# Kernel tuning notes

Hardware: AMD Instinct MI355X
Metric: run time of the kernel (lower is better)

## Reference

```python
import jax, jax.numpy as jnp
import numpy as np

N = 50000      # nodes
E = 800000     # edges (avg degree 16)
F_IN = 64      # node_features (== GENConv out, so no input projection)
H = 64         # hidden
EXP = 2 * H    # GENConv MLP expansion dim = 128
D2 = F_IN + H  # dense-block concat dim = SAGEConv in = 128
EPS_MSG = 1e-7 # GENConv message eps
BN_EPS = 1e-5


def setup_inputs() -> dict:
    key = jax.random.key(0)
    ks = jax.random.split(key, 16)
    g = lambda k, shape, fan: jax.random.normal(k, shape, jnp.float32) / np.sqrt(fan)
    return {
        "x": jax.random.normal(ks[0], (N, F_IN), jnp.float32),
        "edge_index": jax.random.randint(ks[1], (2, E), 0, N, jnp.int32),
        # GENConv MLP: Linear(64,128) -> BatchNorm(128) -> ReLU -> Linear(128,64)
        "W1": g(ks[2], (H, EXP), H), "b1": jnp.zeros((EXP,), jnp.float32),
        "gamma": jnp.ones((EXP,), jnp.float32), "beta": jnp.zeros((EXP,), jnp.float32),
        "W2": g(ks[3], (EXP, H), EXP), "b2": jnp.zeros((H,), jnp.float32),
        # SAGEConv project Linear(128,128), lin_l Linear(128,64), lin_r Linear(128,64,bias=False)
        "Wp": g(ks[4], (D2, D2), D2), "bp": jnp.zeros((D2,), jnp.float32),
        "Wl": g(ks[5], (D2, H), D2), "bl": jnp.zeros((H,), jnp.float32),
        "Wr": g(ks[6], (D2, H), D2),
        # fc Linear(64,1)
        "Wf": g(ks[7], (H, 1), H), "bf": jnp.zeros((1,), jnp.float32),
    }


def _forward(x, W1, b1, gamma, beta, W2, b2, Wp, bp, Wl, bl, Wr, Wf, bf, src, dst):
    n = x.shape[0]
    # ---- GENConv(aggr='softmax', t=1.0): msg = relu(x_j) + eps -------------
    msg = jax.nn.relu(x[src]) + EPS_MSG                       # [E, H]
    mmax = jax.ops.segment_max(msg, dst, num_segments=n)      # per-dst, per-feature max
    mmax = jax.lax.stop_gradient(jnp.where(jnp.isfinite(mmax), mmax, 0.0))
    e = jnp.exp(msg - mmax[dst])                              # t = 1.0
    denom = jax.ops.segment_sum(e, dst, num_segments=n)
    numer = jax.ops.segment_sum(e * msg, dst, num_segments=n)
    agg = numer / jnp.where(denom > 0, denom, 1.0)            # softmax aggregation
    out = agg + x                                             # residual with x_dst
    # GENConv MLP (BatchNorm in training mode: batch stats, biased var)
    h = out @ W1 + b1
    mu = h.mean(axis=0)
    var = h.var(axis=0)
    h = (h - mu) * jax.lax.rsqrt(var + BN_EPS) * gamma + beta
    h = jax.nn.relu(h) @ W2 + b2                              # [N, H]
    # ---- DeepGCNLayer block='dense': concat input ---------------------------
    x2 = jnp.concatenate([x, h], axis=-1)                     # [N, F_IN+H]
    x2 = jax.nn.sigmoid(x2)                                   # self.relu = Sigmoid()
    # ---- SAGEConv(project=True, aggr=DeepSetsAggregation()==sum) -----------
    xp = jax.nn.relu(x2 @ Wp + bp)                            # projected source feats
    aggr = jax.ops.segment_sum(xp[src], dst, num_segments=n)  # DeepSets w/o nns = sum
    out2 = aggr @ Wl + bl + x2 @ Wr                           # root uses UNprojected x2
    out2 = jax.nn.sigmoid(out2)
    logits = out2 @ Wf + bf                                   # [N, 1]
    probs = jax.nn.sigmoid(logits)                            # training branch
    return probs, logits


def reference(x, edge_index, W1, b1, gamma, beta, W2, b2, Wp, bp, Wl, bl, Wr, Wf, bf):
    src, dst = edge_index[0], edge_index[1]
    return _forward(x, W1, b1, gamma, beta, W2, b2, Wp, bp, Wl, bl, Wr, Wf, bf, src, dst)
```

## Files before the change

kernel.cpp:

```cpp
#include <hip/hip_runtime.h>

#define F_IN 64
#define HID 64
#define EXPD 128
#define D2 128
#define MAXDEG 64
#define NBW 128
#define NB 391
#define BINCAP 2400
#define EPT 32

typedef __attribute__((ext_vector_type(8))) short bf16x8;
typedef __attribute__((ext_vector_type(4))) float f32x4;

__device__ __forceinline__ float sigmoidf_(float x) {
    return 1.0f / (1.0f + __expf(-x));
}
__device__ __forceinline__ unsigned bf16rne_(float f) {
    unsigned u = __float_as_uint(f);
    return (u + 0x7FFFu + ((u >> 16) & 1u)) >> 16;
}
__device__ __forceinline__ float bf16tof_(unsigned u16) {
    return __uint_as_float(u16 << 16);
}

__global__ __launch_bounds__(256) void k_bin(const int* __restrict__ ei,
                                             int* __restrict__ binCount,
                                             unsigned* __restrict__ binned,
                                             const float* __restrict__ x,
                                             unsigned short* __restrict__ x16,
                                             const float* __restrict__ W1,
                                             const float* __restrict__ W2,
                                             const float* __restrict__ Wp,
                                             const float* __restrict__ Wl,
                                             const float* __restrict__ Wr,
                                             short* __restrict__ dst,
                                             int nE, int n, int nbinb) {
    int b = blockIdx.x;
    if (b < nbinb) {
        __shared__ int hist[NB];
        __shared__ int base[NB];
        int tid = threadIdx.x;
        for (int i = tid; i < NB; i += 256) hist[i] = 0;
        __syncthreads();
        unsigned ed[EPT];
        unsigned short rk[EPT];
        int e0 = b * (256 * EPT);
#pragma unroll
        for (int j = 0; j < EPT; ++j) {
            int e = e0 + j * 256 + tid;
            if (e < nE) {
                unsigned s = (unsigned)ei[e];
                unsigned d = (unsigned)ei[nE + e];
                ed[j] = s | (d << 16);
                rk[j] = (unsigned short)atomicAdd(&hist[d >> 7], 1);
            }
        }
        __syncthreads();
        for (int i = tid; i < NB; i += 256) {
            int h = hist[i];
            base[i] = h > 0 ? atomicAdd(&binCount[i], h) : 0;
        }
        __syncthreads();
#pragma unroll
        for (int j = 0; j < EPT; ++j) {
            int e = e0 + j * 256 + tid;
            if (e < nE) {
                int bin = (ed[j] >> 16) >> 7;
                int pos = base[bin] + (int)rk[j];
                if (pos < BINCAP) binned[(size_t)bin * BINCAP + pos] = ed[j];
            }
        }
        return;
    }
    b -= nbinb;
    if (b < 192) {
        int e = b * 256 + threadIdx.x;
        const float* src;
        int K, N, base2;
        if (e < 8192)       { src = W1; K = 64;  N = 128; base2 = 0; }
        else if (e < 16384) { src = W2; K = 128; N = 64;  base2 = 8192; }
        else if (e < 32768) { src = Wp; K = 128; N = 128; base2 = 16384; }
        else if (e < 40960) { src = Wl; K = 128; N = 64;  base2 = 32768; }
        else                { src = Wr; K = 128; N = 64;  base2 = 40960; }
        int le = e - base2;
        int j = le & 7;
        int lane = (le >> 3) & 63;
        int n16 = lane & 15, q = lane >> 4;
        int rest = le >> 9;
        int KC = K / 32;
        int kc = rest % KC, nt = rest / KC;
        int k = kc * 32 + q * 8 + j;
        int col = nt * 16 + n16;
        dst[e] = (short)bf16rne_(src[(size_t)k * N + col]);
        return;
    }
    int i0 = (b - 192) * 1024 + threadIdx.x * 4;
    if (i0 < n * F_IN) {
        float4 v = *(const float4*)(x + i0);
        uint2 pk;
        pk.x = bf16rne_(v.x) | (bf16rne_(v.y) << 16);
        pk.y = bf16rne_(v.z) | (bf16rne_(v.w) << 16);
        *(uint2*)(x16 + i0) = pk;
    }
}

__global__ __launch_bounds__(256) void k_csr(const int* __restrict__ binCount,
                                             const unsigned* __restrict__ binned,
                                             int* __restrict__ counts,
                                             unsigned short* __restrict__ csr, int n) {
    __shared__ unsigned short lcsr[NBW * MAXDEG];
    __shared__ int lcnt[NBW];
    int b = blockIdx.x;
    int tid = threadIdx.x;
    if (tid < NBW) lcnt[tid] = 0;
    __syncthreads();
    int cnt = binCount[b];
    cnt = cnt < BINCAP ? cnt : BINCAP;
    const unsigned* src = binned + (size_t)b * BINCAP;
    for (int i = tid; i < cnt; i += 256) {
        unsigned u = src[i];
        int dl = (int)(u >> 16) - b * NBW;
        int slot = atomicAdd(&lcnt[dl], 1);
        if (slot < MAXDEG) lcsr[dl * MAXDEG + slot] = (unsigned short)(u & 0xFFFF);
    }
    __syncthreads();
    int nodebase = b * NBW;
    if (tid < NBW && nodebase + tid < n) counts[nodebase + tid] = lcnt[tid];
    int nrows = n - nodebase;
    nrows = nrows < NBW ? nrows : NBW;
    int nu4 = nrows * 8;
    uint4* dstrow = (uint4*)(csr + (size_t)nodebase * MAXDEG);
    for (int idx = tid; idx < nu4; idx += 256) dstrow[idx] = ((const uint4*)lcsr)[idx];
}

__global__ __launch_bounds__(256) void k_gen(const unsigned short* __restrict__ x16,
                                             const int* __restrict__ counts,
                                             const unsigned short* __restrict__ csr,
                                             unsigned short* __restrict__ gen16, int n) {
    const unsigned* x32 = (const unsigned*)x16;
    int wid = threadIdx.x >> 6;
    int lane = threadIdx.x & 63;
    int H = lane >> 5, f2 = lane & 31;
    int v = blockIdx.x * 4 + wid;
    if (v >= n) return;
    int deg = counts[v];
    deg = deg > MAXDEG ? MAXDEG : deg;
    int idx = 0;
    if (lane < deg) idx = (int)csr[(size_t)v * MAXDEG + lane];
    float d0 = 0.f, d1 = 0.f, n0 = 0.f, n1 = 0.f;
    int i = 0;
    for (; i + 8 <= deg; i += 8) {
        int sA = __shfl(idx, i + 0 + H, 64);
        int sB = __shfl(idx, i + 2 + H, 64);
        int sC = __shfl(idx, i + 4 + H, 64);
        int sD = __shfl(idx, i + 6 + H, 64);
        unsigned uA = x32[(size_t)sA * 32 + f2];
        unsigned uB = x32[(size_t)sB * 32 + f2];
        unsigned uC = x32[(size_t)sC * 32 + f2];
        unsigned uD = x32[(size_t)sD * 32 + f2];
#pragma unroll
        for (int t = 0; t < 4; ++t) {
            unsigned u = t == 0 ? uA : t == 1 ? uB : t == 2 ? uC : uD;
            float m0 = fmaxf(bf16tof_(u & 0xFFFF), 0.f) + 1e-7f;
            float m1 = fmaxf(bf16tof_(u >> 16), 0.f) + 1e-7f;
            float e0 = __expf(m0), e1 = __expf(m1);
            d0 += e0; d1 += e1;
            n0 = fmaf(e0, m0, n0);
            n1 = fmaf(e1, m1, n1);
        }
    }
    for (; i + 2 <= deg; i += 2) {
        int s = __shfl(idx, i + H, 64);
        unsigned u = x32[(size_t)s * 32 + f2];
        float m0 = fmaxf(bf16tof_(u & 0xFFFF), 0.f) + 1e-7f;
        float m1 = fmaxf(bf16tof_(u >> 16), 0.f) + 1e-7f;
        float e0 = __expf(m0), e1 = __expf(m1);
        d0 += e0; d1 += e1;
        n0 = fmaf(e0, m0, n0);
        n1 = fmaf(e1, m1, n1);
    }
    if (i < deg) {
        int s = __shfl(idx, i, 64);
        if (H == 0) {
            unsigned u = x32[(size_t)s * 32 + f2];
            float m0 = fmaxf(bf16tof_(u & 0xFFFF), 0.f) + 1e-7f;
            float m1 = fmaxf(bf16tof_(u >> 16), 0.f) + 1e-7f;
            float e0 = __expf(m0), e1 = __expf(m1);
            d0 += e0; d1 += e1;
            n0 = fmaf(e0, m0, n0);
            n1 = fmaf(e1, m1, n1);
        }
    }
    d0 += __shfl_xor(d0, 32, 64);
    d1 += __shfl_xor(d1, 32, 64);
    n0 += __shfl_xor(n0, 32, 64);
    n1 += __shfl_xor(n1, 32, 64);
    if (H == 0) {
        float a0 = (deg > 0) ? (n0 / d0) : 0.f;
        float a1 = (deg > 0) ? (n1 / d1) : 0.f;
        unsigned xv = x32[(size_t)v * 32 + f2];
        float r0 = a0 + bf16tof_(xv & 0xFFFF);
        float r1 = a1 + bf16tof_(xv >> 16);
        ((unsigned*)gen16)[(size_t)v * 32 + f2] =
            bf16rne_(r0) | (bf16rne_(r1) << 16);
    }
}

__global__ __launch_bounds__(256) void k_gemm1(const unsigned short* __restrict__ gen16,
                                               const short* __restrict__ Wf,
                                               const float* __restrict__ b1,
                                               unsigned short* __restrict__ h16,
                                               float* __restrict__ bnsums, int n) {
    __shared__ short As[64 * 64];
    __shared__ float bnred[256];
    int tid = threadIdx.x;
    int rblk = blockIdx.x * 64;
    if (tid < 256) bnred[tid] = 0.f;
#pragma unroll
    for (int it = 0; it < 2; ++it) {
        int c = it * 256 + tid;
        int rr = c & 63, q8 = c >> 6;
        int gr = rblk + rr;
        gr = gr < n ? gr : n - 1;
        uint4 v = *(const uint4*)(gen16 + (size_t)gr * F_IN + q8 * 8);
        int slot = ((rr >> 4) * 2 + (q8 >> 2)) * 64 + (q8 & 3) * 16 + (rr & 15);
        *(uint4*)(As + slot * 8) = v;
    }
    __syncthreads();
    int L = tid & 63, w = tid >> 6;
    int q = L >> 4, n16 = L & 15;
    int mt_base = (w & 1) * 2;
    int nt_base = (w >> 1) * 4;
    f32x4 acc[2][4];
#pragma unroll
    for (int mt = 0; mt < 2; ++mt)
#pragma unroll
        for (int nt = 0; nt < 4; ++nt) acc[mt][nt] = (f32x4){0.f, 0.f, 0.f, 0.f};
#pragma unroll
    for (int kc = 0; kc < 2; ++kc) {
        bf16x8 a0 = *(const bf16x8*)(As + (((mt_base + 0) * 2 + kc) * 64 + L) * 8);
        bf16x8 a1 = *(const bf16x8*)(As + (((mt_base + 1) * 2 + kc) * 64 + L) * 8);
#pragma unroll
        for (int nt = 0; nt < 4; ++nt) {
            bf16x8 b = *(const bf16x8*)(Wf + (size_t)(((nt_base + nt) * 2 + kc) * 64 + L) * 8);
            acc[0][nt] = __builtin_amdgcn_mfma_f32_16x16x32_bf16(a0, b, acc[0][nt], 0, 0, 0);
            acc[1][nt] = __builtin_amdgcn_mfma_f32_16x16x32_bf16(a1, b, acc[1][nt], 0, 0, 0);
        }
    }
#pragma unroll
    for (int nt = 0; nt < 4; ++nt) {
        int col = (nt_base + nt) * 16 + n16;
        float bv = b1[col];
        float s = 0.f, s2 = 0.f;
#pragma unroll
        for (int mt = 0; mt < 2; ++mt)
#pragma unroll
            for (int r = 0; r < 4; ++r) {
                int row = rblk + (w & 1) * 32 + mt * 16 + q * 4 + r;
                float hv = acc[mt][nt][r] + bv;
                if (row < n) {
                    h16[(size_t)row * EXPD + col] = (unsigned short)bf16rne_(hv);
                    s += hv;
                    s2 = fmaf(hv, hv, s2);
                }
            }
        s += __shfl_xor(s, 16, 64);
        s += __shfl_xor(s, 32, 64);
        s2 += __shfl_xor(s2, 16, 64);
        s2 += __shfl_xor(s2, 32, 64);
        if (q == 0) {
            atomicAdd(&bnred[col], s);
            atomicAdd(&bnred[128 + col], s2);
        }
    }
    __syncthreads();
    if (tid < 256) atomicAdd(&bnsums[tid], bnred[tid]);
}

__global__ __launch_bounds__(256) void k_mlp2a(const unsigned short* __restrict__ h16,
                                               const float* __restrict__ bnsums,
                                               const float* __restrict__ gamma,
                                               const float* __restrict__ beta,
                                               const short* __restrict__ Wf,
                                               const float* __restrict__ b2,
                                               const unsigned short* __restrict__ x16,
                                               unsigned short* __restrict__ x2_16,
                                               float inv_n, int n) {
    __shared__ short As[128 * 128];
    __shared__ float ssl[256];
    int tid = threadIdx.x;
    int rblk = blockIdx.x * 128;
    if (tid < 128) {
        float mu = bnsums[tid] * inv_n;
        float var = fmaf(-mu, mu, bnsums[128 + tid] * inv_n);
        float rs = rsqrtf(fmaxf(var, 0.f) + 1e-5f);
        float scale = gamma[tid] * rs;
        ssl[tid] = scale;
        ssl[128 + tid] = fmaf(-mu, scale, beta[tid]);
    }
    __syncthreads();
#pragma unroll
    for (int it = 0; it < 8; ++it) {
        int c = it * 256 + tid;
        int rr = c & 127, q8 = c >> 7;
        int gr = rblk + rr;
        gr = gr < n ? gr : n - 1;
        uint4 v = *(const uint4*)(h16 + (size_t)gr * EXPD + q8 * 8);
        float4 sc1 = *(const float4*)(ssl + q8 * 8);
        float4 sc2 = *(const float4*)(ssl + q8 * 8 + 4);
        float4 sh1 = *(const float4*)(ssl + 128 + q8 * 8);
        float4 sh2 = *(const float4*)(ssl + 128 + q8 * 8 + 4);
        float o0 = fmaxf(fmaf(bf16tof_(v.x & 0xFFFF), sc1.x, sh1.x), 0.f);
        float o1 = fmaxf(fmaf(bf16tof_(v.x >> 16),    sc1.y, sh1.y), 0.f);
        float o2 = fmaxf(fmaf(bf16tof_(v.y & 0xFFFF), sc1.z, sh1.z), 0.f);
        float o3 = fmaxf(fmaf(bf16tof_(v.y >> 16),    sc1.w, sh1.w), 0.f);
        float o4 = fmaxf(fmaf(bf16tof_(v.z & 0xFFFF), sc2.x, sh2.x), 0.f);
        float o5 = fmaxf(fmaf(bf16tof_(v.z >> 16),    sc2.y, sh2.y), 0.f);
        float o6 = fmaxf(fmaf(bf16tof_(v.w & 0xFFFF), sc2.z, sh2.z), 0.f);
        float o7 = fmaxf(fmaf(bf16tof_(v.w >> 16),    sc2.w, sh2.w), 0.f);
        uint4 pk;
        pk.x = bf16rne_(o0) | (bf16rne_(o1) << 16);
        pk.y = bf16rne_(o2) | (bf16rne_(o3) << 16);
        pk.z = bf16rne_(o4) | (bf16rne_(o5) << 16);
        pk.w = bf16rne_(o6) | (bf16rne_(o7) << 16);
        int slot = ((rr >> 4) * 4 + (q8 >> 2)) * 64 + (q8 & 3) * 16 + (rr & 15);
        *(uint4*)(As + slot * 8) = pk;
    }
    __syncthreads();
    int L = tid & 63, w = tid >> 6;
    int q = L >> 4, n16 = L & 15;
    int mt_base = w * 2;
    f32x4 acc[2][4];
#pragma unroll
    for (int mt = 0; mt < 2; ++mt)
#pragma unroll
        for (int nt = 0; nt < 4; ++nt) acc[mt][nt] = (f32x4){0.f, 0.f, 0.f, 0.f};
#pragma unroll
    for (int kc = 0; kc < 4; ++kc) {
        bf16x8 a0 = *(const bf16x8*)(As + (((mt_base + 0) * 4 + kc) * 64 + L) * 8);
        bf16x8 a1 = *(const bf16x8*)(As + (((mt_base + 1) * 4 + kc) * 64 + L) * 8);
#pragma unroll
        for (int nt = 0; nt < 4; ++nt) {
            bf16x8 b = *(const bf16x8*)(Wf + (size_t)((nt * 4 + kc) * 64 + L) * 8);
            acc[0][nt] = __builtin_amdgcn_mfma_f32_16x16x32_bf16(a0, b, acc[0][nt], 0, 0, 0);
            acc[1][nt] = __builtin_amdgcn_mfma_f32_16x16x32_bf16(a1, b, acc[1][nt], 0, 0, 0);
        }
    }
#pragma unroll
    for (int it = 0; it < 8; ++it) {
        int i = it * 256 + tid;
        int rr = i >> 4, c4 = i & 15;
        int row = rblk + rr;
        if (row < n) {
            uint2 xv = ((const uint2*)x16)[(size_t)row * 16 + c4];
            float s0 = sigmoidf_(bf16tof_(xv.x & 0xFFFF));
            float s1 = sigmoidf_(bf16tof_(xv.x >> 16));
            float s2 = sigmoidf_(bf16tof_(xv.y & 0xFFFF));
            float s3 = sigmoidf_(bf16tof_(xv.y >> 16));
            uint2 pk;
            pk.x = bf16rne_(s0) | (bf16rne_(s1) << 16);
            pk.y = bf16rne_(s2) | (bf16rne_(s3) << 16);
            *(uint2*)(x2_16 + (size_t)row * D2 + c4 * 4) = pk;
        }
    }
#pragma unroll
    for (int nt = 0; nt < 4; ++nt) {
        int col = nt * 16 + n16;
        float bv = b2[col];
#pragma unroll
        for (int mt = 0; mt < 2; ++mt)
#pragma unroll
            for (int r = 0; r < 4; ++r) {
                int row = rblk + w * 32 + mt * 16 + q * 4 + r;
                if (row < n)
                    x2_16[(size_t)row * D2 + 64 + col] =
                        (unsigned short)bf16rne_(sigmoidf_(acc[mt][nt][r] + bv));
            }
    }
}

__global__ __launch_bounds__(256) void k_mlp2b(const unsigned short* __restrict__ x2_16,
                                               const short* __restrict__ Wfp,
                                               const short* __restrict__ Wfl,
                                               const float* __restrict__ bp,
                                               unsigned short* __restrict__ yp16, int n) {
    __shared__ short As[64 * 128];
    int tid = threadIdx.x;
    int rblk = blockIdx.x * 64;
#pragma unroll
    for (int it = 0; it < 4; ++it) {
        int c = it * 256 + tid;
        int rr = c & 63, q8 = c >> 6;
        int gr = rblk + rr;
        gr = gr < n ? gr : n - 1;
        uint4 v = *(const uint4*)(x2_16 + (size_t)gr * D2 + q8 * 8);
        int slot = ((rr >> 4) * 4 + (q8 >> 2)) * 64 + (q8 & 3) * 16 + (rr & 15);
        *(uint4*)(As + slot * 8) = v;
    }
    __syncthreads();
    int L = tid & 63, w = tid >> 6;
    int q = L >> 4, n16 = L & 15;
    int mt_base = (w & 1) * 2;
    int nt_base = (w >> 1) * 4;
    f32x4 acc[2][4];
#pragma unroll
    for (int mt = 0; mt < 2; ++mt)
#pragma unroll
        for (int nt = 0; nt < 4; ++nt) acc[mt][nt] = (f32x4){0.f, 0.f, 0.f, 0.f};
#pragma unroll
    for (int kc = 0; kc < 4; ++kc) {
        bf16x8 a0 = *(const bf16x8*)(As + (((mt_base + 0) * 4 + kc) * 64 + L) * 8);
        bf16x8 a1 = *(const bf16x8*)(As + (((mt_base + 1) * 4 + kc) * 64 + L) * 8);
#pragma unroll
        for (int nt = 0; nt < 4; ++nt) {
            bf16x8 b = *(const bf16x8*)(Wfp + (size_t)(((nt_base + nt) * 4 + kc) * 64 + L) * 8);
            acc[0][nt] = __builtin_amdgcn_mfma_f32_16x16x32_bf16(a0, b, acc[0][nt], 0, 0, 0);
            acc[1][nt] = __builtin_amdgcn_mfma_f32_16x16x32_bf16(a1, b, acc[1][nt], 0, 0, 0);
        }
    }
    __syncthreads();
#pragma unroll
    for (int nt = 0; nt < 4; ++nt) {
        int kk = (nt_base + nt) * 16 + n16;
        float bv = bp[kk];
        int q8b = kk >> 3, jb = kk & 7;
#pragma unroll
        for (int mt = 0; mt < 2; ++mt)
#pragma unroll
            for (int r = 0; r < 4; ++r) {
                int rr2 = (w & 1) * 32 + mt * 16 + q * 4 + r;
                float xv = fmaxf(acc[mt][nt][r] + bv, 0.f);
                int slot = ((rr2 >> 4) * 4 + (q8b >> 2)) * 64 + (q8b & 3) * 16 + (rr2 & 15);
                As[slot * 8 + jb] = (short)bf16rne_(xv);
            }
    }
    __syncthreads();
    f32x4 acc2[4];
#pragma unroll
    for (int nt = 0; nt < 4; ++nt) acc2[nt] = (f32x4){0.f, 0.f, 0.f, 0.f};
#pragma unroll
    for (int kc = 0; kc < 4; ++kc) {
        bf16x8 a = *(const bf16x8*)(As + ((w * 4 + kc) * 64 + L) * 8);
#pragma unroll
        for (int nt = 0; nt < 4; ++nt) {
            bf16x8 b = *(const bf16x8*)(Wfl + (size_t)((nt * 4 + kc) * 64 + L) * 8);
            acc2[nt] = __builtin_amdgcn_mfma_f32_16x16x32_bf16(a, b, acc2[nt], 0, 0, 0);
        }
    }
#pragma unroll
    for (int nt = 0; nt < 4; ++nt) {
        int col = nt * 16 + n16;
#pragma unroll
        for (int r = 0; r < 4; ++r) {
            int row = rblk + w * 16 + q * 4 + r;
            if (row < n)
                yp16[(size_t)row * HID + col] = (unsigned short)bf16rne_(acc2[nt][r]);
        }
    }
}

__global__ __launch_bounds__(256) void k_sage(const unsigned short* __restrict__ yp16,
                                              const int* __restrict__ counts,
                                              const unsigned short* __restrict__ csr,
                                              unsigned short* __restrict__ aggr16, int n) {
    const unsigned* yp32 = (const unsigned*)yp16;
    int wid = threadIdx.x >> 6;
    int lane = threadIdx.x & 63;
    int H = lane >> 5, f2 = lane & 31;
    int v = blockIdx.x * 4 + wid;
    if (v >= n) return;
    int deg = counts[v];
    deg = deg > MAXDEG ? MAXDEG : deg;
    int idx = 0;
    if (lane < deg) idx = (int)csr[(size_t)v * MAXDEG + lane];
    float a0 = 0.f, a1 = 0.f;
    int i = 0;
    for (; i + 8 <= deg; i += 8) {
        int sA = __shfl(idx, i + 0 + H, 64);
        int sB = __shfl(idx, i + 2 + H, 64);
        int sC = __shfl(idx, i + 4 + H, 64);
        int sD = __shfl(idx, i + 6 + H, 64);
        unsigned uA = yp32[(size_t)sA * 32 + f2];
        unsigned uB = yp32[(size_t)sB * 32 + f2];
        unsigned uC = yp32[(size_t)sC * 32 + f2];
        unsigned uD = yp32[(size_t)sD * 32 + f2];
        a0 += bf16tof_(uA & 0xFFFF) + bf16tof_(uB & 0xFFFF) +
              bf16tof_(uC & 0xFFFF) + bf16tof_(uD & 0xFFFF);
        a1 += bf16tof_(uA >> 16) + bf16tof_(uB >> 16) +
              bf16tof_(uC >> 16) + bf16tof_(uD >> 16);
    }
    for (; i + 2 <= deg; i += 2) {
        int s = __shfl(idx, i + H, 64);
        unsigned u = yp32[(size_t)s * 32 + f2];
        a0 += bf16tof_(u & 0xFFFF);
        a1 += bf16tof_(u >> 16);
    }
    if (i < deg) {
        int s = __shfl(idx, i, 64);
        if (H == 0) {
            unsigned u = yp32[(size_t)s * 32 + f2];
            a0 += bf16tof_(u & 0xFFFF);
            a1 += bf16tof_(u >> 16);
        }
    }
    a0 += __shfl_xor(a0, 32, 64);
    a1 += __shfl_xor(a1, 32, 64);
    if (H == 0)
        ((unsigned*)aggr16)[(size_t)v * 32 + f2] = bf16rne_(a0) | (bf16rne_(a1) << 16);
}

__global__ __launch_bounds__(256) void k_final(const unsigned short* __restrict__ aggr16,
                                               const unsigned short* __restrict__ x2_16,
                                               const short* __restrict__ Wfr,
                                               const float* __restrict__ bl,
                                               const float* __restrict__ Wfv,
                                               const float* __restrict__ bf,
                                               float* __restrict__ out, int n) {
    __shared__ short As[128 * 128];
    int tid = threadIdx.x;
    int rblk = blockIdx.x * 128;
#pragma unroll
    for (int it = 0; it < 8; ++it) {
        int c = it * 256 + tid;
        int rr = c & 127, q8 = c >> 7;
        int gr = rblk + rr;
        gr = gr < n ? gr : n - 1;
        uint4 v = *(const uint4*)(x2_16 + (size_t)gr * D2 + q8 * 8);
        int slot = ((rr >> 4) * 4 + (q8 >> 2)) * 64 + (q8 & 3) * 16 + (rr & 15);
        *(uint4*)(As + slot * 8) = v;
    }
    __syncthreads();
    int L = tid & 63, w = tid >> 6;
    int q = L >> 4, n16 = L & 15;
    int mt_base = w * 2;
    f32x4 acc[2][4];
#pragma unroll
    for (int mt = 0; mt < 2; ++mt)
#pragma unroll
        for (int nt = 0; nt < 4; ++nt) acc[mt][nt] = (f32x4){0.f, 0.f, 0.f, 0.f};
#pragma unroll
    for (int kc = 0; kc < 4; ++kc) {
        bf16x8 a0 = *(const bf16x8*)(As + (((mt_base + 0) * 4 + kc) * 64 + L) * 8);
        bf16x8 a1 = *(const bf16x8*)(As + (((mt_base + 1) * 4 + kc) * 64 + L) * 8);
#pragma unroll
        for (int nt = 0; nt < 4; ++nt) {
            bf16x8 b = *(const bf16x8*)(Wfr + (size_t)((nt * 4 + kc) * 64 + L) * 8);
            acc[0][nt] = __builtin_amdgcn_mfma_f32_16x16x32_bf16(a0, b, acc[0][nt], 0, 0, 0);
            acc[1][nt] = __builtin_amdgcn_mfma_f32_16x16x32_bf16(a1, b, acc[1][nt], 0, 0, 0);
        }
    }
    float blv[4], wfv[4];
#pragma unroll
    for (int nt = 0; nt < 4; ++nt) {
        blv[nt] = bl[nt * 16 + n16];
        wfv[nt] = Wfv[nt * 16 + n16];
    }
    float bf0 = bf[0];
#pragma unroll
    for (int mt = 0; mt < 2; ++mt)
#pragma unroll
        for (int r = 0; r < 4; ++r) {
            int row = rblk + w * 32 + mt * 16 + q * 4 + r;
            int rowc = row < n ? row : n - 1;
            float t = 0.f;
#pragma unroll
            for (int nt = 0; nt < 4; ++nt) {
                float ag = bf16tof_(aggr16[(size_t)rowc * HID + nt * 16 + n16]);
                t = fmaf(sigmoidf_(acc[mt][nt][r] + blv[nt] + ag), wfv[nt], t);
            }
            t += __shfl_xor(t, 1, 64);
            t += __shfl_xor(t, 2, 64);
            t += __shfl_xor(t, 4, 64);
            t += __shfl_xor(t, 8, 64);
            if (n16 == 0 && row < n) {
                float lg = t + bf0;
                out[row] = sigmoidf_(lg);
                out[n + row] = lg;
            }
        }
}

extern "C" void kernel_launch(void* const* d_in, const int* in_sizes, int n_in,
                              void* d_out, int out_size, void* d_ws, size_t ws_size,
                              hipStream_t stream) {
    const float* x     = (const float*)d_in[0];
    const int*   ei    = (const int*)d_in[1];
    const float* W1    = (const float*)d_in[2];
    const float* b1    = (const float*)d_in[3];
    const float* gamma = (const float*)d_in[4];
    const float* beta  = (const float*)d_in[5];
    const float* W2    = (const float*)d_in[6];
    const float* b2    = (const float*)d_in[7];
    const float* Wp    = (const float*)d_in[8];
    const float* bp    = (const float*)d_in[9];
    const float* Wl    = (const float*)d_in[10];
    const float* bl    = (const float*)d_in[11];
    const float* Wr    = (const float*)d_in[12];
    const float* Wfv   = (const float*)d_in[13];
    const float* bf    = (const float*)d_in[14];
    const int n = in_sizes[0] / F_IN;
    const int e = in_sizes[1] / 2;

    char* ws = (char*)d_ws;
    size_t off = 0;
    auto alloc = [&](size_t bytes) -> void* {
        void* p = (void*)(ws + off);
        off += (bytes + 255) & ~(size_t)255;
        return p;
    };
    float*          bnsums   = (float*)alloc(256 * 4 + NB * 4);
    int*            binCount = (int*)((char*)bnsums + 1024);
    int*            counts   = (int*)alloc((size_t)n * 4);
    unsigned short* csr      = (unsigned short*)alloc((size_t)n * MAXDEG * 2);
    unsigned*       binned   = (unsigned*)alloc((size_t)NB * BINCAP * 4);
    unsigned short* x16      = (unsigned short*)alloc((size_t)n * F_IN * 2);
    unsigned short* gen16    = (unsigned short*)alloc((size_t)n * F_IN * 2);
    unsigned short* h16      = (unsigned short*)alloc((size_t)n * EXPD * 2);
    unsigned short* x2_16    = (unsigned short*)alloc((size_t)n * D2 * 2);
    unsigned short* yp16     = (unsigned short*)alloc((size_t)n * HID * 2);
    unsigned short* aggr16   = (unsigned short*)alloc((size_t)n * HID * 2);
    short*          wfrag    = (short*)alloc(49152 * 2);

    float* out = (float*)d_out;
    const int nb64  = (n + 63) / 64;
    const int nb128 = (n + 127) / 128;
    const int nb4   = (n + 3) / 4;
    const int nbinb = (e + 256 * EPT - 1) / (256 * EPT);
    const int nfp = nbinb + 192 + ((n * F_IN + 1023) / 1024);

    hipMemsetAsync(bnsums, 0, 1024 + NB * 4, stream);

    k_bin<<<nfp, 256, 0, stream>>>(ei, binCount, binned, x, x16, W1, W2, Wp, Wl,
                                   Wr, wfrag, e, n, nbinb);
    k_csr<<<NB, 256, 0, stream>>>(binCount, binned, counts, csr, n);
    k_gen<<<nb4, 256, 0, stream>>>(x16, counts, csr, gen16, n);
    k_gemm1<<<nb64, 256, 0, stream>>>(gen16, wfrag, b1, h16, bnsums, n);
    k_mlp2a<<<nb128, 256, 0, stream>>>(h16, bnsums, gamma, beta, wfrag + 8192, b2,
                                       x16, x2_16, 1.0f / (float)n, n);
    k_mlp2b<<<nb64, 256, 0, stream>>>(x2_16, wfrag + 16384, wfrag + 32768, bp,
                                      yp16, n);
    k_sage<<<nb4, 256, 0, stream>>>(yp16, counts, csr, aggr16, n);
    k_final<<<nb128, 256, 0, stream>>>(aggr16, x2_16, wfrag + 40960, bl, Wfv, bf,
                                       out, n);
}
```

Measured before the change: 232.7 us.

## Fuse GENConv aggregation into GEMM1 and merge MLP2 with SAGE projection

The softmax gather-aggregation is moved into the first GEMM kernel, so each block aggregates its 64 rows straight into shared memory and the gen16 round trip through global memory goes away. The second MLP GEMM, the sigmoid concat and the SAGE projection/lin_l GEMMs are merged into one kernel that keeps x2 in shared memory instead of re-reading it. This removes two launches and intermediate traffic. The cost is fewer blocks doing the gather (64 rows per block with 16 serial nodes per wave) and a larger per-block register and LDS footprint, which may reduce latency hiding.

```diff
diff --git a/kernel.cpp b/kernel.cpp
--- a/kernel.cpp
+++ b/kernel.cpp
@@ -134,55 +134,52 @@
     for (int idx = tid; idx < nu4; idx += 256) dstrow[idx] = ((const uint4*)lcsr)[idx];
 }
 
-__global__ __launch_bounds__(256) void k_gen(const unsigned short* __restrict__ x16,
-                                             const int* __restrict__ counts,
-                                             const unsigned short* __restrict__ csr,
-                                             unsigned short* __restrict__ gen16, int n) {
+__global__ __launch_bounds__(256) void k_gengemm1(const unsigned short* __restrict__ x16,
+                                                  const int* __restrict__ counts,
+                                                  const unsigned short* __restrict__ csr,
+                                                  const short* __restrict__ Wf,
+                                                  const float* __restrict__ b1,
+                                                  unsigned short* __restrict__ h16,
+                                                  float* __restrict__ bnsums, int n) {
+    __shared__ short As[64 * 64];
+    __shared__ float bnred[256];
     const unsigned* x32 = (const unsigned*)x16;
-    int wid = threadIdx.x >> 6;
-    int lane = threadIdx.x & 63;
-    int H = lane >> 5, f2 = lane & 31;
-    int v = blockIdx.x * 4 + wid;
-    if (v >= n) return;
-    int deg = counts[v];
-    deg = deg > MAXDEG ? MAXDEG : deg;
-    int idx = 0;
-    if (lane < deg) idx = (int)csr[(size_t)v * MAXDEG + lane];
-    float d0 = 0.f, d1 = 0.f, n0 = 0.f, n1 = 0.f;
-    int i = 0;
-    for (; i + 8 <= deg; i += 8) {
-        int sA = __shfl(idx, i + 0 + H, 64);
-        int sB = __shfl(idx, i + 2 + H, 64);
-        int sC = __shfl(idx, i + 4 + H, 64);
-        int sD = __shfl(idx, i + 6 + H, 64);
-        unsigned uA = x32[(size_t)sA * 32 + f2];
-        unsigned uB = x32[(size_t)sB * 32 + f2];
-        unsigned uC = x32[(size_t)sC * 32 + f2];
-        unsigned uD = x32[(size_t)sD * 32 + f2];
-#pragma unroll
-        for (int t = 0; t < 4; ++t) {
-            unsigned u = t == 0 ? uA : t == 1 ? uB : t == 2 ? uC : uD;
-            float m0 = fmaxf(bf16tof_(u & 0xFFFF), 0.f) + 1e-7f;
-            float m1 = fmaxf(bf16tof_(u >> 16), 0.f) + 1e-7f;
-            float e0 = __expf(m0), e1 = __expf(m1);
-            d0 += e0; d1 += e1;
-            n0 = fmaf(e0, m0, n0);
-            n1 = fmaf(e1, m1, n1);
-        }
-    }
-    for (; i + 2 <= deg; i += 2) {
-        int s = __shfl(idx, i + H, 64);
-        unsigned u = x32[(size_t)s * 32 + f2];
-        float m0 = fmaxf(bf16tof_(u & 0xFFFF), 0.f) + 1e-7f;
-        float m1 = fmaxf(bf16tof_(u >> 16), 0.f) + 1e-7f;
-        float e0 = __expf(m0), e1 = __expf(m1);
-        d0 += e0; d1 += e1;
-        n0 = fmaf(e0, m0, n0);
-        n1 = fmaf(e1, m1, n1);
-    }
-    if (i < deg) {
-        int s = __shfl(idx, i, 64);
-        if (H == 0) {
+    int tid = threadIdx.x;
+    int rblk = blockIdx.x * 64;
+    if (tid < 256) bnred[tid] = 0.f;
+    int L = tid & 63, w = tid >> 6;
+    int H = L >> 5, f2 = L & 31;
+    for (int t = 0; t < 16; ++t) {
+        int vv = rblk + w * 16 + t;
+        int v = vv < n ? vv : n - 1;
+        int deg = counts[v];
+        deg = deg > MAXDEG ? MAXDEG : deg;
+        int idx = 0;
+        if (L < deg) idx = (int)csr[(size_t)v * MAXDEG + L];
+        float d0 = 0.f, d1 = 0.f, n0 = 0.f, n1 = 0.f;
+        int i = 0;
+        for (; i + 8 <= deg; i += 8) {
+            int sA = __shfl(idx, i + 0 + H, 64);
+            int sB = __shfl(idx, i + 2 + H, 64);
+            int sC = __shfl(idx, i + 4 + H, 64);
+            int sD = __shfl(idx, i + 6 + H, 64);
+            unsigned uA = x32[(size_t)sA * 32 + f2];
+            unsigned uB = x32[(size_t)sB * 32 + f2];
+            unsigned uC = x32[(size_t)sC * 32 + f2];
+            unsigned uD = x32[(size_t)sD * 32 + f2];
+#pragma unroll
+            for (int tt = 0; tt < 4; ++tt) {
+                unsigned u = tt == 0 ? uA : tt == 1 ? uB : tt == 2 ? uC : uD;
+                float m0 = fmaxf(bf16tof_(u & 0xFFFF), 0.f) + 1e-7f;
+                float m1 = fmaxf(bf16tof_(u >> 16), 0.f) + 1e-7f;
+                float e0 = __expf(m0), e1 = __expf(m1);
+                d0 += e0; d1 += e1;
+                n0 = fmaf(e0, m0, n0);
+                n1 = fmaf(e1, m1, n1);
+            }
+        }
+        for (; i + 2 <= deg; i += 2) {
+            int s = __shfl(idx, i + H, 64);
             unsigned u = x32[(size_t)s * 32 + f2];
             float m0 = fmaxf(bf16tof_(u & 0xFFFF), 0.f) + 1e-7f;
             float m1 = fmaxf(bf16tof_(u >> 16), 0.f) + 1e-7f;
@@ -191,44 +188,35 @@
             n0 = fmaf(e0, m0, n0);
             n1 = fmaf(e1, m1, n1);
         }
-    }
-    d0 += __shfl_xor(d0, 32, 64);
-    d1 += __shfl_xor(d1, 32, 64);
-    n0 += __shfl_xor(n0, 32, 64);
-    n1 += __shfl_xor(n1, 32, 64);
-    if (H == 0) {
-        float a0 = (deg > 0) ? (n0 / d0) : 0.f;
-        float a1 = (deg > 0) ? (n1 / d1) : 0.f;
-        unsigned xv = x32[(size_t)v * 32 + f2];
-        float r0 = a0 + bf16tof_(xv & 0xFFFF);
-        float r1 = a1 + bf16tof_(xv >> 16);
-        ((unsigned*)gen16)[(size_t)v * 32 + f2] =
-            bf16rne_(r0) | (bf16rne_(r1) << 16);
-    }
-}
-
-__global__ __launch_bounds__(256) void k_gemm1(const unsigned short* __restrict__ gen16,
-                                               const short* __restrict__ Wf,
-                                               const float* __restrict__ b1,
-                                               unsigned short* __restrict__ h16,
-                                               float* __restrict__ bnsums, int n) {
-    __shared__ short As[64 * 64];
-    __shared__ float bnred[256];
-    int tid = threadIdx.x;
-    int rblk = blockIdx.x * 64;
-    if (tid < 256) bnred[tid] = 0.f;
-#pragma unroll
-    for (int it = 0; it < 2; ++it) {
-        int c = it * 256 + tid;
-        int rr = c & 63, q8 = c >> 6;
-        int gr = rblk + rr;
-        gr = gr < n ? gr : n - 1;
-        uint4 v = *(const uint4*)(gen16 + (size_t)gr * F_IN + q8 * 8);
-        int slot = ((rr >> 4) * 2 + (q8 >> 2)) * 64 + (q8 & 3) * 16 + (rr & 15);
-        *(uint4*)(As + slot * 8) = v;
-    }
-    __syncthreads();
-    int L = tid & 63, w = tid >> 6;
+        if (i < deg) {
+            int s = __shfl(idx, i, 64);
+            if (H == 0) {
+                unsigned u = x32[(size_t)s * 32 + f2];
+                float m0 = fmaxf(bf16tof_(u & 0xFFFF), 0.f) + 1e-7f;
+                float m1 = fmaxf(bf16tof_(u >> 16), 0.f) + 1e-7f;
+                float e0 = __expf(m0), e1 = __expf(m1);
+                d0 += e0; d1 += e1;
+                n0 = fmaf(e0, m0, n0);
+                n1 = fmaf(e1, m1, n1);
+            }
+        }
+        d0 += __shfl_xor(d0, 32, 64);
+        d1 += __shfl_xor(d1, 32, 64);
+        n0 += __shfl_xor(n0, 32, 64);
+        n1 += __shfl_xor(n1, 32, 64);
+        if (H == 0) {
+            float a0 = (deg > 0) ? (n0 / d0) : 0.f;
+            float a1 = (deg > 0) ? (n1 / d1) : 0.f;
+            unsigned xv = x32[(size_t)v * 32 + f2];
+            float r0 = a0 + bf16tof_(xv & 0xFFFF);
+            float r1 = a1 + bf16tof_(xv >> 16);
+            int q8 = f2 >> 2;
+            int j = (2 * f2) & 7;
+            int slot = (w * 2 + (q8 >> 2)) * 64 + (q8 & 3) * 16 + t;
+            *(unsigned*)(As + slot * 8 + j) = bf16rne_(r0) | (bf16rne_(r1) << 16);
+        }
+    }
+    __syncthreads();
     int q = L >> 4, n16 = L & 15;
     int mt_base = (w & 1) * 2;
     int nt_base = (w >> 1) * 4;
@@ -278,15 +266,19 @@
     if (tid < 256) atomicAdd(&bnsums[tid], bnred[tid]);
 }
 
-__global__ __launch_bounds__(256) void k_mlp2a(const unsigned short* __restrict__ h16,
-                                               const float* __restrict__ bnsums,
-                                               const float* __restrict__ gamma,
-                                               const float* __restrict__ beta,
-                                               const short* __restrict__ Wf,
-                                               const float* __restrict__ b2,
-                                               const unsigned short* __restrict__ x16,
-                                               unsigned short* __restrict__ x2_16,
-                                               float inv_n, int n) {
+__global__ __launch_bounds__(256) void k_mlp2(const unsigned short* __restrict__ h16,
+                                              const float* __restrict__ bnsums,
+                                              const float* __restrict__ gamma,
+                                              const float* __restrict__ beta,
+                                              const short* __restrict__ Wf2,
+                                              const float* __restrict__ b2,
+                                              const unsigned short* __restrict__ x16,
+                                              const short* __restrict__ Wfp,
+                                              const short* __restrict__ Wfl,
+                                              const float* __restrict__ bp,
+                                              unsigned short* __restrict__ x2_16,
+                                              unsigned short* __restrict__ yp16,
+                                              float inv_n, int n) {
     __shared__ short As[128 * 128];
     __shared__ float ssl[256];
     int tid = threadIdx.x;
@@ -330,7 +322,6 @@
     __syncthreads();
     int L = tid & 63, w = tid >> 6;
     int q = L >> 4, n16 = L & 15;
-    int mt_base = w * 2;
     f32x4 acc[2][4];
 #pragma unroll
     for (int mt = 0; mt < 2; ++mt)
@@ -338,125 +329,114 @@
         for (int nt = 0; nt < 4; ++nt) acc[mt][nt] = (f32x4){0.f, 0.f, 0.f, 0.f};
 #pragma unroll
     for (int kc = 0; kc < 4; ++kc) {
-        bf16x8 a0 = *(const bf16x8*)(As + (((mt_base + 0) * 4 + kc) * 64 + L) * 8);
-        bf16x8 a1 = *(const bf16x8*)(As + (((mt_base + 1) * 4 + kc) * 64 + L) * 8);
+        bf16x8 a0 = *(const bf16x8*)(As + (((w * 2 + 0) * 4 + kc) * 64 + L) * 8);
+        bf16x8 a1 = *(const bf16x8*)(As + (((w * 2 + 1) * 4 + kc) * 64 + L) * 8);
 #pragma unroll
         for (int nt = 0; nt < 4; ++nt) {
-            bf16x8 b = *(const bf16x8*)(Wf + (size_t)((nt * 4 + kc) * 64 + L) * 8);
+            bf16x8 b = *(const bf16x8*)(Wf2 + (size_t)((nt * 4 + kc) * 64 + L) * 8);
             acc[0][nt] = __builtin_amdgcn_mfma_f32_16x16x32_bf16(a0, b, acc[0][nt], 0, 0, 0);
             acc[1][nt] = __builtin_amdgcn_mfma_f32_16x16x32_bf16(a1, b, acc[1][nt], 0, 0, 0);
         }
     }
+    __syncthreads();
 #pragma unroll
     for (int it = 0; it < 8; ++it) {
         int i = it * 256 + tid;
         int rr = i >> 4, c4 = i & 15;
-        int row = rblk + rr;
-        if (row < n) {
-            uint2 xv = ((const uint2*)x16)[(size_t)row * 16 + c4];
-            float s0 = sigmoidf_(bf16tof_(xv.x & 0xFFFF));
-            float s1 = sigmoidf_(bf16tof_(xv.x >> 16));
-            float s2 = sigmoidf_(bf16tof_(xv.y & 0xFFFF));
-            float s3 = sigmoidf_(bf16tof_(xv.y >> 16));
-            uint2 pk;
-            pk.x = bf16rne_(s0) | (bf16rne_(s1) << 16);
-            pk.y = bf16rne_(s2) | (bf16rne_(s3) << 16);
-            *(uint2*)(x2_16 + (size_t)row * D2 + c4 * 4) = pk;
-        }
+        int gr = rblk + rr;
+        int grc = gr < n ? gr : n - 1;
+        uint2 xv = ((const uint2*)x16)[(size_t)grc * 16 + c4];
+        float s0 = sigmoidf_(bf16tof_(xv.x & 0xFFFF));
+        float s1 = sigmoidf_(bf16tof_(xv.x >> 16));
+        float s2 = sigmoidf_(bf16tof_(xv.y & 0xFFFF));
+        float s3 = sigmoidf_(bf16tof_(xv.y >> 16));
+        uint2 pk;
+        pk.x = bf16rne_(s0) | (bf16rne_(s1) << 16);
+        pk.y = bf16rne_(s2) | (bf16rne_(s3) << 16);
+        if (gr < n) *(uint2*)(x2_16 + (size_t)gr * D2 + c4 * 4) = pk;
+        int q8 = c4 >> 1, j = (c4 & 1) * 4;
+        int slot = ((rr >> 4) * 4 + (q8 >> 2)) * 64 + (q8 & 3) * 16 + (rr & 15);
+        *(uint2*)(As + slot * 8 + j) = pk;
     }
 #pragma unroll
     for (int nt = 0; nt < 4; ++nt) {
         int col = nt * 16 + n16;
         float bv = b2[col];
+        int kk = 64 + col;
+        int q8b = kk >> 3, jb = kk & 7;
 #pragma unroll
         for (int mt = 0; mt < 2; ++mt)
 #pragma unroll
             for (int r = 0; r < 4; ++r) {
-                int row = rblk + w * 32 + mt * 16 + q * 4 + r;
+                int rr2 = w * 32 + mt * 16 + q * 4 + r;
+                int row = rblk + rr2;
+                unsigned sv = bf16rne_(sigmoidf_(acc[mt][nt][r] + bv));
                 if (row < n)
-                    x2_16[(size_t)row * D2 + 64 + col] =
-                        (unsigned short)bf16rne_(sigmoidf_(acc[mt][nt][r] + bv));
-            }
-    }
-}
-
-__global__ __launch_bounds__(256) void k_mlp2b(const unsigned short* __restrict__ x2_16,
-                                               const short* __restrict__ Wfp,
-                                               const short* __restrict__ Wfl,
-                                               const float* __restrict__ bp,
-                                               unsigned short* __restrict__ yp16, int n) {
-    __shared__ short As[64 * 128];
-    int tid = threadIdx.x;
-    int rblk = blockIdx.x * 64;
-#pragma unroll
-    for (int it = 0; it < 4; ++it) {
-        int c = it * 256 + tid;
-        int rr = c & 63, q8 = c >> 6;
-        int gr = rblk + rr;
-        gr = gr < n ? gr : n - 1;
-        uint4 v = *(const uint4*)(x2_16 + (size_t)gr * D2 + q8 * 8);
-        int slot = ((rr >> 4) * 4 + (q8 >> 2)) * 64 + (q8 & 3) * 16 + (rr & 15);
-        *(uint4*)(As + slot * 8) = v;
-    }
-    __syncthreads();
-    int L = tid & 63, w = tid >> 6;
-    int q = L >> 4, n16 = L & 15;
-    int mt_base = (w & 1) * 2;
-    int nt_base = (w >> 1) * 4;
-    f32x4 acc[2][4];
+                    x2_16[(size_t)row * D2 + 64 + col] = (unsigned short)sv;
+                int slot = ((rr2 >> 4) * 4 + (q8b >> 2)) * 64 + (q8b & 3) * 16 + (rr2 & 15);
+                As[slot * 8 + jb] = (short)sv;
+            }
+    }
+    __syncthreads();
+    f32x4 accp[2][8];
 #pragma unroll
     for (int mt = 0; mt < 2; ++mt)
 #pragma unroll
-        for (int nt = 0; nt < 4; ++nt) acc[mt][nt] = (f32x4){0.f, 0.f, 0.f, 0.f};
+        for (int nt = 0; nt < 8; ++nt) accp[mt][nt] = (f32x4){0.f, 0.f, 0.f, 0.f};
 #pragma unroll
     for (int kc = 0; kc < 4; ++kc) {
-        bf16x8 a0 = *(const bf16x8*)(As + (((mt_base + 0) * 4 + kc) * 64 + L) * 8);
-        bf16x8 a1 = *(const bf16x8*)(As + (((mt_base + 1) * 4 + kc) * 64 + L) * 8);
-#pragma unroll
-        for (int nt = 0; nt < 4; ++nt) {
-            bf16x8 b = *(const bf16x8*)(Wfp + (size_t)(((nt_base + nt) * 4 + kc) * 64 + L) * 8);
-            acc[0][nt] = __builtin_amdgcn_mfma_f32_16x16x32_bf16(a0, b, acc[0][nt], 0, 0, 0);
-            acc[1][nt] = __builtin_amdgcn_mfma_f32_16x16x32_bf16(a1, b, acc[1][nt], 0, 0, 0);
-        }
-    }
-    __syncthreads();
-#pragma unroll
-    for (int nt = 0; nt < 4; ++nt) {
-        int kk = (nt_base + nt) * 16 + n16;
-        float bv = bp[kk];
-        int q8b = kk >> 3, jb = kk & 7;
+        bf16x8 a0 = *(const bf16x8*)(As + (((w * 2 + 0) * 4 + kc) * 64 + L) * 8);
+        bf16x8 a1 = *(const bf16x8*)(As + (((w * 2 + 1) * 4 + kc) * 64 + L) * 8);
+#pragma unroll
+        for (int nt = 0; nt < 8; ++nt) {
+            bf16x8 b = *(const bf16x8*)(Wfp + (size_t)((nt * 4 + kc) * 64 + L) * 8);
+            accp[0][nt] = __builtin_amdgcn_mfma_f32_16x16x32_bf16(a0, b, accp[0][nt], 0, 0, 0);
+            accp[1][nt] = __builtin_amdgcn_mfma_f32_16x16x32_bf16(a1, b, accp[1][nt], 0, 0, 0);
+        }
+    }
+#pragma unroll
+    for (int nt = 0; nt < 8; ++nt) {
+        int col = nt * 16 + n16;
+        float bv = bp[col];
+        int q8b = col >> 3, jb = col & 7;
 #pragma unroll
         for (int mt = 0; mt < 2; ++mt)
 #pragma unroll
             for (int r = 0; r < 4; ++r) {
-                int rr2 = (w & 1) * 32 + mt * 16 + q * 4 + r;
-                float xv = fmaxf(acc[mt][nt][r] + bv, 0.f);
+                int rr2 = (w * 2 + mt) * 16 + q * 4 + r;
+                float xv = fmaxf(accp[mt][nt][r] + bv, 0.f);
                 int slot = ((rr2 >> 4) * 4 + (q8b >> 2)) * 64 + (q8b & 3) * 16 + (rr2 & 15);
                 As[slot * 8 + jb] = (short)bf16rne_(xv);
             }
     }
-    __syncthreads();
-    f32x4 acc2[4];
-#pragma unroll
-    for (int nt = 0; nt < 4; ++nt) acc2[nt] = (f32x4){0.f, 0.f, 0.f, 0.f};
+    f32x4 acc2[2][4];
+#pragma unroll
+    for (int mt = 0; mt < 2; ++mt)
+#pragma unroll
+        for (int nt = 0; nt < 4; ++nt) acc2[mt][nt] = (f32x4){0.f, 0.f, 0.f, 0.f};
 #pragma unroll
     for (int kc = 0; kc < 4; ++kc) {
-        bf16x8 a = *(const bf16x8*)(As + ((w * 4 + kc) * 64 + L) * 8);
+        bf16x8 a0 = *(const bf16x8*)(As + (((w * 2 + 0) * 4 + kc) * 64 + L) * 8);
+        bf16x8 a1 = *(const bf16x8*)(As + (((w * 2 + 1) * 4 + kc) * 64 + L) * 8);
 #pragma unroll
         for (int nt = 0; nt < 4; ++nt) {
             bf16x8 b = *(const bf16x8*)(Wfl + (size_t)((nt * 4 + kc) * 64 + L) * 8);
-            acc2[nt] = __builtin_amdgcn_mfma_f32_16x16x32_bf16(a, b, acc2[nt], 0, 0, 0);
+            acc2[0][nt] = __builtin_amdgcn_mfma_f32_16x16x32_bf16(a0, b, acc2[0][nt], 0, 0, 0);
+            acc2[1][nt] = __builtin_amdgcn_mfma_f32_16x16x32_bf16(a1, b, acc2[1][nt], 0, 0, 0);
         }
     }
 #pragma unroll
     for (int nt = 0; nt < 4; ++nt) {
         int col = nt * 16 + n16;
 #pragma unroll
-        for (int r = 0; r < 4; ++r) {
-            int row = rblk + w * 16 + q * 4 + r;
-            if (row < n)
-                yp16[(size_t)row * HID + col] = (unsigned short)bf16rne_(acc2[nt][r]);
-        }
+        for (int mt = 0; mt < 2; ++mt)
+#pragma unroll
+            for (int r = 0; r < 4; ++r) {
+                int row = rblk + (w * 2 + mt) * 16 + q * 4 + r;
+                if (row < n)
+                    yp16[(size_t)row * HID + col] =
+                        (unsigned short)bf16rne_(acc2[mt][nt][r]);
+            }
     }
 }
 
@@ -615,7 +595,6 @@
     unsigned short* csr      = (unsigned short*)alloc((size_t)n * MAXDEG * 2);
     unsigned*       binned   = (unsigned*)alloc((size_t)NB * BINCAP * 4);
     unsigned short* x16      = (unsigned short*)alloc((size_t)n * F_IN * 2);
-    unsigned short* gen16    = (unsigned short*)alloc((size_t)n * F_IN * 2);
     unsigned short* h16      = (unsigned short*)alloc((size_t)n * EXPD * 2);
     unsigned short* x2_16    = (unsigned short*)alloc((size_t)n * D2 * 2);
     unsigned short* yp16     = (unsigned short*)alloc((size_t)n * HID * 2);
@@ -634,12 +613,11 @@
     k_bin<<<nfp, 256, 0, stream>>>(ei, binCount, binned, x, x16, W1, W2, Wp, Wl,
                                    Wr, wfrag, e, n, nbinb);
     k_csr<<<NB, 256, 0, stream>>>(binCount, binned, counts, csr, n);
-    k_gen<<<nb4, 256, 0, stream>>>(x16, counts, csr, gen16, n);
-    k_gemm1<<<nb64, 256, 0, stream>>>(gen16, wfrag, b1, h16, bnsums, n);
-    k_mlp2a<<<nb128, 256, 0, stream>>>(h16, bnsums, gamma, beta, wfrag + 8192, b2,
-                                       x16, x2_16, 1.0f / (float)n, n);
-    k_mlp2b<<<nb64, 256, 0, stream>>>(x2_16, wfrag + 16384, wfrag + 32768, bp,
-                                      yp16, n);
+    k_gengemm1<<<nb64, 256, 0, stream>>>(x16, counts, csr, wfrag, b1, h16,
+                                         bnsums, n);
+    k_mlp2<<<nb128, 256, 0, stream>>>(h16, bnsums, gamma, beta, wfrag + 8192, b2,
+                                      x16, wfrag + 16384, wfrag + 32768, bp,
+                                      x2_16, yp16, 1.0f / (float)n, n);
     k_sage<<<nb4, 256, 0, stream>>>(yp16, counts, csr, aggr16, n);
     k_final<<<nb128, 256, 0, stream>>>(aggr16, x2_16, wfrag + 40960, bl, Wfv, bf,
                                        out, n);
```

Result: slower. 246.1 us (+5.8%).
